# Kernel tuning notes

Hardware: AMD Instinct MI355X
Metric: run time of the kernel (lower is better)

Reference implementation:

```python
import jax, jax.numpy as jnp
import numpy as np

B, S, HMODEL = 2, 4096, 2048
NH, HD, K = 16, 128, 4
RMS_EPS = 1e-5
L2_EPS = 1e-6


def setup_inputs() -> dict:
    key = jax.random.key(0)
    ks = jax.random.split(key, 10)
    def p(k, shape, std=0.02):
        return jax.random.normal(k, shape, jnp.float32) * std
    return {
        "x": jax.random.normal(ks[0], (B, S, HMODEL), jnp.float32),
        "Wq": p(ks[1], (NH * HD, HMODEL)),
        "Wk": p(ks[2], (NH * HD, HMODEL)),
        "Wv": p(ks[3], (NH * HD, HMODEL)),
        "Wb": p(ks[4], (NH, HMODEL)),
        "Wo": p(ks[5], (HMODEL, NH * HD)),
        "conv_q": p(ks[6], (NH * HD, K), 0.3),
        "conv_k": p(ks[7], (NH * HD, K), 0.3),
        "conv_v": p(ks[8], (NH * HD, K), 0.3),
        "rms_w": jnp.ones((HD,), jnp.float32),
    }


def causal_conv_silu(x, w):
    # depthwise causal conv1d: x [B,S,C], w [C,K]; out[t] = sum_i w[:,i]*x[t-K+1+i]
    Kw = w.shape[1]
    xp = jnp.pad(x, ((0, 0), (Kw - 1, 0), (0, 0)))
    out = sum(w[:, i] * xp[:, i:i + x.shape[1], :] for i in range(Kw))
    return jax.nn.silu(out)


def l2norm(x):
    return x * jax.lax.rsqrt(jnp.sum(x * x, axis=-1, keepdims=True) + L2_EPS)


def reference(x, Wq, Wk, Wv, Wb, Wo, conv_q, conv_k, conv_v, rms_w):
    b, s, _ = x.shape
    nh = Wb.shape[0]
    hd = Wq.shape[0] // nh

    q = causal_conv_silu(x @ Wq.T, conv_q)
    k = causal_conv_silu(x @ Wk.T, conv_k)
    v = causal_conv_silu(x @ Wv.T, conv_v)

    q = q.reshape(b, s, nh, hd)
    k = k.reshape(b, s, nh, hd)
    v = v.reshape(b, s, nh, hd)
    beta = jax.nn.sigmoid(x @ Wb.T)  # [B,S,NH]

    # qk l2 norm in kernel + default scale d_k^-0.5 on q
    q = l2norm(q) * (hd ** -0.5)
    k = l2norm(k)

    # delta rule recurrence: state [B,NH,HD,HD] (d_k x d_v)
    qT = jnp.moveaxis(q, 1, 0)  # [S,B,NH,HD]
    kT = jnp.moveaxis(k, 1, 0)
    vT = jnp.moveaxis(v, 1, 0)
    bT = jnp.moveaxis(beta, 1, 0)  # [S,B,NH]

    def step(state, inp):
        qt, kt, vt, bt = inp
        pred = jnp.einsum('bhd,bhdv->bhv', kt, state)
        delta = bt[..., None] * (vt - pred)
        state = state + jnp.einsum('bhd,bhv->bhdv', kt, delta)
        ot = jnp.einsum('bhd,bhdv->bhv', qt, state)
        return state, ot

    s0 = jnp.zeros((b, nh, hd, hd), x.dtype)
    _, o = jax.lax.scan(step, s0, (qT, kT, vT, bT))
    o = jnp.moveaxis(o, 0, 1)  # [B,S,NH,HD]

    # RMSNorm over head_dim
    o = o * jax.lax.rsqrt(jnp.mean(o * o, axis=-1, keepdims=True) + RMS_EPS) * rms_w

    o = o.reshape(b, s, nh * hd) @ Wo.T
    return o
```

## Files before the change

### kernel.cpp

```cpp
#include <hip/hip_runtime.h>

#define DI __device__ __forceinline__

constexpr int Bb = 2, Ss = 4096, Hm = 2048, NHh = 16, HDd = 128;
constexpr int ROWS = Bb * Ss;
constexpr int QKVN = 3 * Hm;
constexpr int CC = 64;
constexpr int NC = Ss / CC;

typedef __bf16 bf16x8 __attribute__((ext_vector_type(8)));
typedef float f32x4 __attribute__((ext_vector_type(4)));

DI unsigned short f2bf(float f) {
  unsigned int u = __float_as_uint(f);
  u = u + 0x7FFFu + ((u >> 16) & 1u);
  return (unsigned short)(u >> 16);
}
DI float bf2f(unsigned int u) { return __uint_as_float(u << 16); }
DI void ld_bf8(const unsigned short* p, float* f) {
  uint4 u = *(const uint4*)p;
  f[0] = bf2f(u.x & 0xffffu); f[1] = bf2f(u.x >> 16);
  f[2] = bf2f(u.y & 0xffffu); f[3] = bf2f(u.y >> 16);
  f[4] = bf2f(u.z & 0xffffu); f[5] = bf2f(u.z >> 16);
  f[6] = bf2f(u.w & 0xffffu); f[7] = bf2f(u.w >> 16);
}

DI void gld16(const unsigned short* g, unsigned short* l) {
  __builtin_amdgcn_global_load_lds(
      (const __attribute__((address_space(1))) unsigned int*)g,
      (__attribute__((address_space(3))) unsigned int*)l, 16, 0, 0);
}

DI void bar_lds() {
  asm volatile("s_waitcnt lgkmcnt(0)" ::: "memory");
  __builtin_amdgcn_s_barrier();
}

__global__ void cast_x_k(const float* __restrict__ x, unsigned short* __restrict__ xb) {
  int i = blockIdx.x * 256 + threadIdx.x;
  float4 f = ((const float4*)x)[i];
  ushort4 u;
  u.x = f2bf(f.x); u.y = f2bf(f.y); u.z = f2bf(f.z); u.w = f2bf(f.w);
  ((ushort4*)xb)[i] = u;
}

__global__ void cast_w_k(const float* __restrict__ Wq, const float* __restrict__ Wk,
                         const float* __restrict__ Wv, const float* __restrict__ Wo,
                         unsigned short* __restrict__ wqkv, unsigned short* __restrict__ wo) {
  const int W1 = Hm * Hm;
  int idx = blockIdx.x * 256 + threadIdx.x;
  for (int r = 0; r < 4; r++) {
    int i = idx + r * W1;
    if (i < W1)            wqkv[i] = f2bf(Wq[i]);
    else if (i < 2 * W1)   wqkv[i] = f2bf(Wk[i - W1]);
    else if (i < 3 * W1)   wqkv[i] = f2bf(Wv[i - 2 * W1]);
    else                   wo[i - 3 * W1] = f2bf(Wo[i - 3 * W1]);
  }
}

DI bf16x8 ldsw(const unsigned short* base, int r, int c16) {
  return *(const bf16x8*)&base[r * 64 + ((c16 ^ (r & 7)) << 3)];
}

template <bool BF16_OUT>
__global__ __launch_bounds__(512) void gemm256(const unsigned short* __restrict__ A,
                                               const unsigned short* __restrict__ Bm,
                                               void* __restrict__ Cout,
                                               int M, int N, int Kd) {
  __shared__ __align__(16) unsigned short As[3][16384];
  __shared__ __align__(16) unsigned short Bs[2][16384];
  int tid = threadIdx.x;
  int wave = tid >> 6, lane = tid & 63;
  int lm = lane & 15, lq = lane >> 4;
  int wm = (wave >> 2) * 128, wn = (wave & 3) * 64;

  int nx = N >> 8;
  int nwg = gridDim.x * gridDim.y;
  int lin = blockIdx.x + gridDim.x * blockIdx.y;
  int cpx = nwg >> 3;
  int swz = (lin & 7) * cpx + (lin >> 3);
  int bn = (swz % nx) << 8, bm = (swz / nx) << 8;

  int NT = Kd >> 6;
  int rsub = lane >> 3;
  int csw = ((lane & 7) ^ rsub) << 3;

  auto stageA = [&](int buf, int half, int ts) {
    int ksrc = (ts < NT ? ts : NT - 1) << 6;
#pragma unroll
    for (int i = 0; i < 2; i++) {
      int blk = wave * 2 + i;
      int r = half * 128 + blk * 8 + rsub;
      gld16(&A[(size_t)(bm + r) * Kd + ksrc + csw], &As[buf][half * 8192 + blk * 512]);
    }
  };
  auto stageB = [&](int buf, int half, int ts) {
    int ksrc = (ts < NT ? ts : NT - 1) << 6;
#pragma unroll
    for (int i = 0; i < 2; i++) {
      int blk = wave * 2 + i;
      int r = half * 128 + blk * 8 + rsub;
      gld16(&Bm[(size_t)(bn + r) * Kd + ksrc + csw], &Bs[buf][half * 8192 + blk * 512]);
    }
  };

  f32x4 acc[8][4] = {};
  bf16x8 a[4][2], b[4][2];

  stageA(0, 0, 0); stageA(0, 1, 0); stageB(0, 0, 0); stageB(0, 1, 0);
  stageA(1, 0, 1); stageA(1, 1, 1); stageB(1, 0, 1); stageB(1, 1, 1);
  asm volatile("s_waitcnt vmcnt(8)" ::: "memory");
  __builtin_amdgcn_s_barrier();
#pragma unroll
  for (int fi = 0; fi < 4; fi++)
#pragma unroll
    for (int kk = 0; kk < 2; kk++)
      a[fi][kk] = ldsw(As[0], wm + fi * 16 + lm, kk * 4 + lq);
#pragma unroll
  for (int fj = 0; fj < 2; fj++)
#pragma unroll
    for (int kk = 0; kk < 2; kk++)
      b[fj][kk] = ldsw(Bs[0], wn + fj * 16 + lm, kk * 4 + lq);

  int cur_a = 0, cur_b = 0;
  for (int t = 0; t < NT; t++) {
    const unsigned short* Ac = As[cur_a];
    const unsigned short* Bc = Bs[cur_b];
    int nxt_a = cur_a == 2 ? 0 : cur_a + 1;
    const unsigned short* An = As[nxt_a];
    const unsigned short* Bn = Bs[cur_b ^ 1];
    int ap2 = cur_a == 0 ? 2 : cur_a - 1;

    asm volatile("" ::: "memory");
    __builtin_amdgcn_s_barrier();
    asm volatile("s_waitcnt lgkmcnt(0)" ::: "memory");
    __builtin_amdgcn_sched_barrier(0);
    __builtin_amdgcn_s_setprio(1);
#pragma unroll
    for (int fj = 0; fj < 2; fj++)
#pragma unroll
      for (int kk = 0; kk < 2; kk++)
        b[2 + fj][kk] = ldsw(Bc, wn + (2 + fj) * 16 + lm, kk * 4 + lq);
#pragma unroll
    for (int kk = 0; kk < 2; kk++)
#pragma unroll
      for (int fi = 0; fi < 4; fi++)
#pragma unroll
        for (int fj = 0; fj < 2; fj++)
          acc[fi][fj] = __builtin_amdgcn_mfma_f32_16x16x32_bf16(a[fi][kk], b[fj][kk], acc[fi][fj], 0, 0, 0);
    __builtin_amdgcn_s_setprio(0);
    stageA(ap2, 0, t + 2);

    asm volatile("" ::: "memory");
    __builtin_amdgcn_s_barrier();
    asm volatile("s_waitcnt lgkmcnt(0)" ::: "memory");
    __builtin_amdgcn_sched_barrier(0);
    __builtin_amdgcn_s_setprio(1);
#pragma unroll
    for (int fi = 0; fi < 4; fi++) {
#pragma unroll
      for (int kk = 0; kk < 2; kk++)
#pragma unroll
        for (int fj = 0; fj < 2; fj++)
          acc[fi][2 + fj] = __builtin_amdgcn_mfma_f32_16x16x32_bf16(a[fi][kk], b[2 + fj][kk], acc[fi][2 + fj], 0, 0, 0);
#pragma unroll
      for (int kk = 0; kk < 2; kk++)
        a[fi][kk] = ldsw(Ac, wm + 64 + fi * 16 + lm, kk * 4 + lq);
    }
    __builtin_amdgcn_s_setprio(0);
    stageA(ap2, 1, t + 2);

    asm volatile("" ::: "memory");
    __builtin_amdgcn_s_barrier();
    asm volatile("s_waitcnt lgkmcnt(0)" ::: "memory");
    __builtin_amdgcn_sched_barrier(0);
    __builtin_amdgcn_s_setprio(1);
#pragma unroll
    for (int kk = 0; kk < 2; kk++)
#pragma unroll
      for (int fi = 0; fi < 4; fi++)
#pragma unroll
        for (int fj = 0; fj < 2; fj++)
          acc[4 + fi][2 + fj] = __builtin_amdgcn_mfma_f32_16x16x32_bf16(a[fi][kk], b[2 + fj][kk], acc[4 + fi][2 + fj], 0, 0, 0);
    __builtin_amdgcn_s_setprio(0);
    stageB(cur_b, 0, t + 2);

    asm volatile("" ::: "memory");
    __builtin_amdgcn_s_barrier();
    asm volatile("s_waitcnt vmcnt(6) lgkmcnt(0)" ::: "memory");
    __builtin_amdgcn_sched_barrier(0);
    asm volatile("" ::: "memory");
    __builtin_amdgcn_s_barrier();
    __builtin_amdgcn_s_setprio(1);
#pragma unroll
    for (int fi = 0; fi < 4; fi++) {
#pragma unroll
      for (int kk = 0; kk < 2; kk++)
#pragma unroll
        for (int fj = 0; fj < 2; fj++)
          acc[4 + fi][fj] = __builtin_amdgcn_mfma_f32_16x16x32_bf16(a[fi][kk], b[fj][kk], acc[4 + fi][fj], 0, 0, 0);
#pragma unroll
      for (int kk = 0; kk < 2; kk++)
        a[fi][kk] = ldsw(An, wm + fi * 16 + lm, kk * 4 + lq);
    }
#pragma unroll
    for (int fj = 0; fj < 2; fj++)
#pragma unroll
      for (int kk = 0; kk < 2; kk++)
        b[fj][kk] = ldsw(Bn, wn + fj * 16 + lm, kk * 4 + lq);
    __builtin_amdgcn_s_setprio(0);
    stageB(cur_b, 1, t + 2);

    cur_a = nxt_a; cur_b ^= 1;
  }

#pragma unroll
  for (int fi = 0; fi < 8; fi++)
#pragma unroll
    for (int fj = 0; fj < 4; fj++) {
      int row = bm + wm + fi * 16 + lq * 4;
      int col = bn + wn + fj * 16 + lm;
#pragma unroll
      for (int r = 0; r < 4; r++) {
        if (BF16_OUT)
          ((unsigned short*)Cout)[(size_t)(row + r) * N + col] = f2bf(acc[fi][fj][r]);
        else
          ((float*)Cout)[(size_t)(row + r) * N + col] = acc[fi][fj][r];
      }
    }
}

__global__ __launch_bounds__(256) void conv_k(const unsigned short* __restrict__ qkvh,
                                              const float* __restrict__ cwq,
                                              const float* __restrict__ cwk,
                                              const float* __restrict__ cwv,
                                              unsigned short* __restrict__ qb,
                                              unsigned short* __restrict__ kb,
                                              unsigned short* __restrict__ vb) {
  __shared__ __align__(16) float sm[32 * 260];
  __shared__ float fac[64];
  int tid = threadIdx.x;
  int cblk = blockIdx.x * 256;
  int s0 = blockIdx.y * 32;
  int z = blockIdx.z;
  int sel = z >> 1, b = z & 1;
  const float* cw = sel == 0 ? cwq : (sel == 1 ? cwk : cwv);
  int c = cblk + tid;
  float4 w = ((const float4*)cw)[c];
  const unsigned short* in = qkvh + (size_t)b * Ss * QKVN + sel * Hm + c;
  float x0 = (s0 >= 3) ? bf2f(in[(size_t)(s0 - 3) * QKVN]) : 0.f;
  float x1 = (s0 >= 2) ? bf2f(in[(size_t)(s0 - 2) * QKVN]) : 0.f;
  float x2 = (s0 >= 1) ? bf2f(in[(size_t)(s0 - 1) * QKVN]) : 0.f;
  for (int si = 0; si < 32; si++) {
    float x3 = bf2f(in[(size_t)(s0 + si) * QKVN]);
    float a = w.x * x0 + w.y * x1 + w.z * x2 + w.w * x3;
    sm[si * 260 + tid] = a / (1.f + __expf(-a));
    x0 = x1; x1 = x2; x2 = x3;
  }
  __syncthreads();
  if (sel < 2) {
    int si = tid >> 3, p = tid & 7;
    const float* row = &sm[si * 260 + p * 32];
    float ss = 0.f;
#pragma unroll
    for (int j = 0; j < 32; j += 4) {
      float4 v4 = *(const float4*)(row + j);
      ss += v4.x * v4.x + v4.y * v4.y + v4.z * v4.z + v4.w * v4.w;
    }
    ss += __shfl_xor(ss, 1);
    ss += __shfl_xor(ss, 2);
    float f = rsqrtf(ss + 1e-6f);
    if (sel == 0) f *= 0.08838834764831845f;
    if ((p & 3) == 0) fac[si * 2 + (p >> 2)] = f;
  }
  __syncthreads();
  unsigned short* outp = sel == 0 ? qb : (sel == 1 ? kb : vb);
  int hl = tid >> 7;
  for (int si = 0; si < 32; si++) {
    float val = sm[si * 260 + tid];
    if (sel < 2) val *= fac[si * 2 + hl];
    outp[(size_t)(b * Ss + s0 + si) * Hm + cblk + tid] = f2bf(val);
  }
}

__global__ __launch_bounds__(256) void beta_k(const float* __restrict__ x,
                                              const float* __restrict__ Wbm,
                                              float* __restrict__ beta) {
  int wid = threadIdx.x >> 6, lane = threadIdx.x & 63;
  int row = blockIdx.x * 4 + wid;
  int h = lane & 15, part = lane >> 4;
  const float* xr = x + (size_t)row * Hm + part * 512;
  const float* wr = Wbm + (size_t)h * Hm + part * 512;
  float acc = 0.f;
  for (int j = 0; j < 512; j += 4) {
    float4 xv = *(const float4*)(xr + j);
    float4 wv = *(const float4*)(wr + j);
    acc += xv.x * wv.x + xv.y * wv.y + xv.z * wv.z + xv.w * wv.w;
  }
  acc += __shfl_xor(acc, 16);
  acc += __shfl_xor(acc, 32);
  if (part == 0) beta[(size_t)row * NHh + h] = 1.f / (1.f + __expf(-acc));
}

__global__ __launch_bounds__(256) void recA_k(const unsigned short* __restrict__ qg,
                                              unsigned short* kg,
                                              const unsigned short* __restrict__ vg,
                                              const float* __restrict__ beta,
                                              unsigned short* __restrict__ Wo_,
                                              unsigned short* __restrict__ Uo,
                                              unsigned short* __restrict__ Kto) {
  __shared__ __align__(16) unsigned short Kc[64 * 136];
  __shared__ __align__(16) unsigned short Qc[64 * 136];
  __shared__ __align__(16) unsigned short Vt[128 * 72];
  __shared__ __align__(16) unsigned short Kt[128 * 72];
  __shared__ __align__(16) unsigned short Xa[64 * 72], Xat[64 * 72];
  __shared__ __align__(16) unsigned short Xb2[64 * 72], Xbt[64 * 72];
  __shared__ __align__(16) unsigned short Pa[64 * 72], Pb[64 * 72];
  __shared__ float bl[64];
  int tid = threadIdx.x;
  int c = blockIdx.x, bh = blockIdx.y;
  int b = bh >> 4, h = bh & 15;
  size_t cid = (size_t)bh * NC + c;
  size_t rowbase = (size_t)b * Ss + (size_t)c * CC;
  int wave = tid >> 6, lane = tid & 63, lm = lane & 15, lq = lane >> 4;

  for (int idx = tid; idx < 1024; idx += 256) {
    int r = idx >> 4, c8 = (idx & 15) * 8;
    *(uint4*)&Kc[r * 136 + c8] = *(const uint4*)&kg[(rowbase + r) * Hm + h * HDd + c8];
    *(uint4*)&Qc[r * 136 + c8] = *(const uint4*)&qg[(rowbase + r) * Hm + h * HDd + c8];
  }
  for (int idx = tid; idx < 8192; idx += 256) {
    int s = idx >> 7, vv = idx & 127;
    Vt[vv * 72 + s] = vg[(rowbase + s) * Hm + h * HDd + vv];
  }
  if (tid < 64) bl[tid] = beta[(rowbase + tid) * NHh + h];
  __syncthreads();

  for (int idx = tid; idx < 8192; idx += 256) {
    int s = idx >> 7, d = idx & 127;
    Kt[d * 72 + s] = Kc[s * 136 + d];
  }
  {
    f32x4 accA[4] = {};
#pragma unroll
    for (int kk = 0; kk < 4; kk++) {
      bf16x8 af = *(const bf16x8*)&Kc[(wave * 16 + lm) * 136 + kk * 32 + lq * 8];
#pragma unroll
      for (int st = 0; st < 4; st++) {
        bf16x8 bfr = *(const bf16x8*)&Kc[(st * 16 + lm) * 136 + kk * 32 + lq * 8];
        accA[st] = __builtin_amdgcn_mfma_f32_16x16x32_bf16(af, bfr, accA[st], 0, 0, 0);
      }
    }
#pragma unroll
    for (int st = 0; st < 4; st++)
#pragma unroll
      for (int r = 0; r < 4; r++) {
        int t = wave * 16 + lq * 4 + r, s = st * 16 + lm;
        float m = (t > s) ? -bl[t] * accA[st][r] : 0.f;
        unsigned short mb = f2bf(m);
        Xa[t * 72 + s] = mb;
        Xat[s * 72 + t] = mb;
        Pa[t * 72 + s] = (t == s) ? f2bf(1.f) : mb;
      }
  }
  {
    f32x4 accQ[4] = {};
#pragma unroll
    for (int kk = 0; kk < 4; kk++) {
      bf16x8 af = *(const bf16x8*)&Qc[(wave * 16 + lm) * 136 + kk * 32 + lq * 8];
#pragma unroll
      for (int st = 0; st < 4; st++) {
        bf16x8 bfr = *(const bf16x8*)&Kc[(st * 16 + lm) * 136 + kk * 32 + lq * 8];
        accQ[st] = __builtin_amdgcn_mfma_f32_16x16x32_bf16(af, bfr, accQ[st], 0, 0, 0);
      }
    }
#pragma unroll
    for (int st = 0; st < 4; st++)
#pragma unroll
      for (int r = 0; r < 4; r++) {
        int t = wave * 16 + lq * 4 + r, s = st * 16 + lm;
        kg[(rowbase + t) * Hm + h * HDd + s] = (s <= t) ? f2bf(accQ[st][r]) : (unsigned short)0;
      }
  }
  __syncthreads();

  unsigned short *X = Xa, *Xt = Xat, *Xn = Xb2, *Xnt = Xbt, *P = Pa, *Pn = Pb;
  for (int lvl = 1; lvl <= 5; lvl++) {
    f32x4 a1[4] = {}, a2[4] = {};
#pragma unroll
    for (int kk = 0; kk < 2; kk++) {
      bf16x8 afx  = *(const bf16x8*)&X[(wave * 16 + lm) * 72 + kk * 32 + lq * 8];
      bf16x8 afxt = *(const bf16x8*)&Xt[(wave * 16 + lm) * 72 + kk * 32 + lq * 8];
#pragma unroll
      for (int st = 0; st < 4; st++) {
        bf16x8 bx  = *(const bf16x8*)&X[(st * 16 + lm) * 72 + kk * 32 + lq * 8];
        bf16x8 bxt = *(const bf16x8*)&Xt[(st * 16 + lm) * 72 + kk * 32 + lq * 8];
        a1[st] = __builtin_amdgcn_mfma_f32_16x16x32_bf16(afx, bxt, a1[st], 0, 0, 0);
        a2[st] = __builtin_amdgcn_mfma_f32_16x16x32_bf16(afxt, bx, a2[st], 0, 0, 0);
      }
    }
#pragma unroll
    for (int st = 0; st < 4; st++)
#pragma unroll
      for (int r = 0; r < 4; r++) {
        int t = wave * 16 + lq * 4 + r, s = st * 16 + lm;
        Xn[t * 72 + s]  = f2bf(a1[st][r]);
        Xnt[t * 72 + s] = f2bf(a2[st][r]);
      }
    __syncthreads();
    f32x4 ap[4];
#pragma unroll
    for (int st = 0; st < 4; st++)
#pragma unroll
      for (int r = 0; r < 4; r++)
        ap[st][r] = bf2f(P[(wave * 16 + lq * 4 + r) * 72 + st * 16 + lm]);
#pragma unroll
    for (int kk = 0; kk < 2; kk++) {
      bf16x8 afp = *(const bf16x8*)&P[(wave * 16 + lm) * 72 + kk * 32 + lq * 8];
#pragma unroll
      for (int st = 0; st < 4; st++) {
        bf16x8 bxnt = *(const bf16x8*)&Xnt[(st * 16 + lm) * 72 + kk * 32 + lq * 8];
        ap[st] = __builtin_amdgcn_mfma_f32_16x16x32_bf16(afp, bxnt, ap[st], 0, 0, 0);
      }
    }
#pragma unroll
    for (int st = 0; st < 4; st++)
#pragma unroll
      for (int r = 0; r < 4; r++) {
        int t = wave * 16 + lq * 4 + r, s = st * 16 + lm;
        Pn[t * 72 + s] = f2bf((lvl == 5) ? ap[st][r] * bl[s] : ap[st][r]);
      }
    unsigned short* tmp;
    tmp = X; X = Xn; Xn = tmp;
    tmp = Xt; Xt = Xnt; Xnt = tmp;
    tmp = P; P = Pn; Pn = tmp;
    __syncthreads();
  }

  for (int idx = tid; idx < 1024; idx += 256) {
    int d = idx >> 3, s8 = (idx & 7) * 8;
    *(uint4*)&Kto[cid * 8192 + d * 64 + s8] = *(const uint4*)&Kt[d * 72 + s8];
  }
  {
    unsigned short* Up = Uo + cid * 8192;
    unsigned short* Wp = Wo_ + cid * 8192;
    f32x4 accU[8] = {}, accW[8] = {};
#pragma unroll
    for (int kk = 0; kk < 2; kk++) {
      bf16x8 af = *(const bf16x8*)&P[(wave * 16 + lm) * 72 + kk * 32 + lq * 8];
#pragma unroll
      for (int nt = 0; nt < 8; nt++) {
        bf16x8 bv = *(const bf16x8*)&Vt[(nt * 16 + lm) * 72 + kk * 32 + lq * 8];
        bf16x8 bk = *(const bf16x8*)&Kt[(nt * 16 + lm) * 72 + kk * 32 + lq * 8];
        accU[nt] = __builtin_amdgcn_mfma_f32_16x16x32_bf16(af, bv, accU[nt], 0, 0, 0);
        accW[nt] = __builtin_amdgcn_mfma_f32_16x16x32_bf16(af, bk, accW[nt], 0, 0, 0);
      }
    }
#pragma unroll
    for (int nt = 0; nt < 8; nt++)
#pragma unroll
      for (int r = 0; r < 4; r++) {
        int t = wave * 16 + lq * 4 + r, n = nt * 16 + lm;
        Up[t * 128 + n] = f2bf(accU[nt][r]);
        Wp[t * 128 + n] = f2bf(accW[nt][r]);
      }
  }
}

__global__ __launch_bounds__(256) void recB_k(const unsigned short* __restrict__ qg,
                                              const unsigned short* __restrict__ atg,
                                              const unsigned short* __restrict__ Wg,
                                              const unsigned short* __restrict__ Ug,
                                              const unsigned short* __restrict__ Ktg,
                                              unsigned short* __restrict__ og) {
  __shared__ __align__(16) unsigned short Wc[64 * 136];
  __shared__ __align__(16) unsigned short Qc[64 * 136];
  __shared__ __align__(16) unsigned short Ktc[128 * 72];
  __shared__ __align__(16) unsigned short Atc[64 * 72];
  __shared__ __align__(16) unsigned short Uc[64 * 24];
  __shared__ __align__(16) unsigned short Dt[16 * 72];
  __shared__ __align__(16) unsigned short Stb[16 * 136];
  __shared__ float St32[16 * 132];
  int tid = threadIdx.x;
  int lin = blockIdx.x + (blockIdx.y << 3);
  int xcd = lin & 7, slot = lin >> 3;
  int vs = slot & 7;
  int bh = xcd + ((slot >> 3) << 3);
  int b = bh >> 4, h = bh & 15, v0 = vs * 16;
  int wave = tid >> 6, lane = tid & 63, lm = lane & 15, lq = lane >> 4;

  for (int i = tid; i < 16 * 132; i += 256) St32[i] = 0.f;
  for (int i = tid; i < 16 * 136; i += 256) Stb[i] = 0;

  {
    size_t cid0 = (size_t)bh * NC;
    size_t rb0 = (size_t)b * Ss;
    const unsigned short* Wp = Wg + cid0 * 8192;
    const unsigned short* Ktp = Ktg + cid0 * 8192;
    const unsigned short* Up = Ug + cid0 * 8192 + v0;
#pragma unroll
    for (int j = 0; j < 4; j++) {
      int idx = tid + j * 256;
      int r = idx >> 4, c8 = (idx & 15) * 8;
      *(uint4*)&Wc[r * 136 + c8] = *(const uint4*)&Wp[r * 128 + c8];
      *(uint4*)&Qc[r * 136 + c8] = *(const uint4*)&qg[(rb0 + r) * Hm + h * HDd + c8];
      int r2 = idx >> 3, d8 = (idx & 7) * 8;
      *(uint4*)&Ktc[r2 * 72 + d8] = *(const uint4*)&Ktp[r2 * 64 + d8];
    }
#pragma unroll
    for (int j = 0; j < 2; j++) {
      int idx = tid + j * 256;
      int t = idx >> 3, s8 = (idx & 7) * 8;
      *(uint4*)&Atc[t * 72 + s8] = *(const uint4*)&atg[(rb0 + t) * Hm + h * HDd + s8];
    }
    if (tid < 128) {
      int t = tid >> 1, c8 = (tid & 1) * 8;
      *(uint4*)&Uc[t * 24 + c8] = *(const uint4*)&Up[t * 128 + c8];
    }
  }
  __syncthreads();

  for (int c = 0; c < NC; c++) {
    size_t rb = (size_t)b * Ss + (size_t)c * CC;
    int cn = (c + 1 < NC) ? c + 1 : c;
    size_t cidn = (size_t)bh * NC + cn;
    size_t rbn = (size_t)b * Ss + (size_t)cn * CC;
    const unsigned short* Wpn = Wg + cidn * 8192;
    const unsigned short* Ktpn = Ktg + cidn * 8192;
    const unsigned short* Upn = Ug + cidn * 8192 + v0;
    uint4 pw[4], pq[4], pk[4], pa[2], pu;
#pragma unroll
    for (int j = 0; j < 4; j++) {
      int idx = tid + j * 256;
      int r = idx >> 4, c8 = (idx & 15) * 8;
      pw[j] = *(const uint4*)&Wpn[r * 128 + c8];
      pq[j] = *(const uint4*)&qg[(rbn + r) * Hm + h * HDd + c8];
      int r2 = idx >> 3, d8 = (idx & 7) * 8;
      pk[j] = *(const uint4*)&Ktpn[r2 * 64 + d8];
    }
#pragma unroll
    for (int j = 0; j < 2; j++) {
      int idx = tid + j * 256;
      int t = idx >> 3, s8 = (idx & 7) * 8;
      pa[j] = *(const uint4*)&atg[(rbn + t) * Hm + h * HDd + s8];
    }
    if (tid < 128) {
      int t = tid >> 1, c8 = (tid & 1) * 8;
      pu = *(const uint4*)&Upn[t * 128 + c8];
    }

    {
      f32x4 accD = {};
#pragma unroll
      for (int kk = 0; kk < 4; kk++) {
        bf16x8 af = *(const bf16x8*)&Wc[(wave * 16 + lm) * 136 + kk * 32 + lq * 8];
        bf16x8 bfr = *(const bf16x8*)&Stb[lm * 136 + kk * 32 + lq * 8];
        accD = __builtin_amdgcn_mfma_f32_16x16x32_bf16(af, bfr, accD, 0, 0, 0);
      }
#pragma unroll
      for (int r = 0; r < 4; r++) {
        int t = wave * 16 + lq * 4 + r;
        float dv = bf2f(Uc[t * 24 + lm]) - accD[r];
        Dt[lm * 72 + t] = f2bf(dv);
      }
    }
    bar_lds();

    f32x4 accO = {};
    f32x4 accP[2] = {};
    {
#pragma unroll
      for (int kk = 0; kk < 4; kk++) {
        bf16x8 af = *(const bf16x8*)&Qc[(wave * 16 + lm) * 136 + kk * 32 + lq * 8];
        bf16x8 bfr = *(const bf16x8*)&Stb[lm * 136 + kk * 32 + lq * 8];
        accO = __builtin_amdgcn_mfma_f32_16x16x32_bf16(af, bfr, accO, 0, 0, 0);
      }
#pragma unroll
      for (int kk = 0; kk < 2; kk++) {
        bf16x8 af = *(const bf16x8*)&Atc[(wave * 16 + lm) * 72 + kk * 32 + lq * 8];
        bf16x8 bfr = *(const bf16x8*)&Dt[lm * 72 + kk * 32 + lq * 8];
        accO = __builtin_amdgcn_mfma_f32_16x16x32_bf16(af, bfr, accO, 0, 0, 0);
        bf16x8 afd = *(const bf16x8*)&Dt[lm * 72 + kk * 32 + lq * 8];
#pragma unroll
        for (int j = 0; j < 2; j++) {
          int dt = wave * 2 + j;
          bf16x8 bk = *(const bf16x8*)&Ktc[(dt * 16 + lm) * 72 + kk * 32 + lq * 8];
          accP[j] = __builtin_amdgcn_mfma_f32_16x16x32_bf16(afd, bk, accP[j], 0, 0, 0);
        }
      }
    }
    bar_lds();

#pragma unroll
    for (int r = 0; r < 4; r++) {
      int t = wave * 16 + lq * 4 + r;
      og[(rb + t) * Hm + h * HDd + v0 + lm] = f2bf(accO[r]);
    }
#pragma unroll
    for (int j = 0; j < 2; j++) {
      int dt = wave * 2 + j;
#pragma unroll
      for (int r = 0; r < 4; r++) {
        int vv = lq * 4 + r, d = dt * 16 + lm;
        float ns = St32[vv * 132 + d] + accP[j][r];
        St32[vv * 132 + d] = ns;
        Stb[vv * 136 + d] = f2bf(ns);
      }
    }
#pragma unroll
    for (int j = 0; j < 4; j++) {
      int idx = tid + j * 256;
      int r = idx >> 4, c8 = (idx & 15) * 8;
      *(uint4*)&Wc[r * 136 + c8] = pw[j];
      *(uint4*)&Qc[r * 136 + c8] = pq[j];
      int r2 = idx >> 3, d8 = (idx & 7) * 8;
      *(uint4*)&Ktc[r2 * 72 + d8] = pk[j];
    }
#pragma unroll
    for (int j = 0; j < 2; j++) {
      int idx = tid + j * 256;
      int t = idx >> 3, s8 = (idx & 7) * 8;
      *(uint4*)&Atc[t * 72 + s8] = pa[j];
    }
    if (tid < 128) {
      int t = tid >> 1, c8 = (tid & 1) * 8;
      *(uint4*)&Uc[t * 24 + c8] = pu;
    }
    bar_lds();
  }
}

__global__ __launch_bounds__(256) void rmsn_k(const unsigned short* __restrict__ o,
                                              const float* __restrict__ rw,
                                              unsigned short* __restrict__ ob) {
  int tid = threadIdx.x;
  size_t rowoff = (size_t)blockIdx.x * Hm + tid * 8;
  float f[8];
  ld_bf8(o + rowoff, f);
  float ss = f[0]*f[0] + f[1]*f[1] + f[2]*f[2] + f[3]*f[3] +
             f[4]*f[4] + f[5]*f[5] + f[6]*f[6] + f[7]*f[7];
  ss += __shfl_xor(ss, 1); ss += __shfl_xor(ss, 2); ss += __shfl_xor(ss, 4); ss += __shfl_xor(ss, 8);
  float sc = rsqrtf(ss * (1.f / 128.f) + 1e-5f);
  int d = (tid & 15) * 8;
  float4 wa = *(const float4*)(rw + d);
  float4 wb = *(const float4*)(rw + d + 4);
  ushort4 u0, u1;
  u0.x = f2bf(f[0] * sc * wa.x); u0.y = f2bf(f[1] * sc * wa.y);
  u0.z = f2bf(f[2] * sc * wa.z); u0.w = f2bf(f[3] * sc * wa.w);
  u1.x = f2bf(f[4] * sc * wb.x); u1.y = f2bf(f[5] * sc * wb.y);
  u1.z = f2bf(f[6] * sc * wb.z); u1.w = f2bf(f[7] * sc * wb.w);
  ((ushort4*)ob)[rowoff / 4] = u0;
  ((ushort4*)ob)[rowoff / 4 + 1] = u1;
}

extern "C" void kernel_launch(void* const* d_in, const int* in_sizes, int n_in,
                              void* d_out, int out_size, void* d_ws, size_t ws_size,
                              hipStream_t stream) {
  const float* x  = (const float*)d_in[0];
  const float* Wq = (const float*)d_in[1];
  const float* Wk = (const float*)d_in[2];
  const float* Wv = (const float*)d_in[3];
  const float* Wb = (const float*)d_in[4];
  const float* Wo = (const float*)d_in[5];
  const float* cq = (const float*)d_in[6];
  const float* ck = (const float*)d_in[7];
  const float* cv = (const float*)d_in[8];
  const float* rw = (const float*)d_in[9];

  unsigned short* xb  = (unsigned short*)d_out;
  unsigned short* vb  = (unsigned short*)d_out + (size_t)ROWS * Hm;
  unsigned short* o_b = (unsigned short*)d_out;
  float* out = (float*)d_out;

  char* ws = (char*)d_ws;
  size_t off = 0;
  auto alloc = [&](size_t bytes) {
    void* p = ws + off;
    off = (off + bytes + 255) & ~(size_t)255;
    return p;
  };
  unsigned short* wqkv = (unsigned short*)alloc((size_t)QKVN * Hm * 2);
  unsigned short* wob  = (unsigned short*)alloc((size_t)Hm * Hm * 2);
  unsigned short* qkvh = (unsigned short*)alloc((size_t)ROWS * QKVN * 2);
  unsigned short* qb   = (unsigned short*)alloc((size_t)ROWS * Hm * 2);
  unsigned short* kb   = (unsigned short*)alloc((size_t)ROWS * Hm * 2);
  float* beta          = (float*)alloc((size_t)ROWS * NHh * 4);
  unsigned short* Wch = qkvh;
  unsigned short* Uch = qkvh + (size_t)2048 * 8192;
  unsigned short* Kth = qkvh + (size_t)2 * 2048 * 8192;
  unsigned short* obb = qkvh;

  cast_x_k<<<ROWS * Hm / 1024, 256, 0, stream>>>(x, xb);
  cast_w_k<<<Hm * Hm / 256, 256, 0, stream>>>(Wq, Wk, Wv, Wo, wqkv, wob);
  gemm256<true><<<dim3(QKVN / 256, ROWS / 256), 512, 0, stream>>>(xb, wqkv, qkvh, ROWS, QKVN, Hm);
  beta_k<<<ROWS / 4, 256, 0, stream>>>(x, Wb, beta);
  conv_k<<<dim3(Hm / 256, Ss / 32, Bb * 3), 256, 0, stream>>>(qkvh, cq, ck, cv, qb, kb, vb);
  recA_k<<<dim3(NC, 32), 256, 0, stream>>>(qb, kb, vb, beta, Wch, Uch, Kth);
  recB_k<<<dim3(8, 32), 256, 0, stream>>>(qb, kb, Wch, Uch, Kth, o_b);
  rmsn_k<<<ROWS, 256, 0, stream>>>(o_b, rw, obb);
  gemm256<false><<<dim3(Hm / 256, ROWS / 256), 512, 0, stream>>>(obb, wob, out, ROWS, Hm, Hm);
}
```

Baseline: 934.0 us.

## Shrink recA shared memory via buffer aliasing to fit two blocks per CU

Replaces the separate shared arrays in recA_k with one aliased byte buffer. Q and transposed V share storage, Kt reuses the X buffers after the doubling loop, and P is updated in place. The row stride drops from 72 to 68, V is staged through registers instead of a strided global gather, the last-level X product is skipped, and the kernel is marked for two blocks per CU via launch_bounds. The goal is higher occupancy and less global and LDS traffic, at the cost of more complex barrier ordering and possible LDS bank conflicts from the 68 stride.

Measured after the change: 1.003 ms. 7.4% more time.

```diff
diff --git a/kernel.cpp b/kernel.cpp
--- a/kernel.cpp
+++ b/kernel.cpp
@@ -302,21 +302,24 @@
   if (part == 0) beta[(size_t)row * NHh + h] = 1.f / (1.f + __expf(-acc));
 }
 
-__global__ __launch_bounds__(256) void recA_k(const unsigned short* __restrict__ qg,
+__global__ __launch_bounds__(256, 2) void recA_k(const unsigned short* __restrict__ qg,
                                               unsigned short* kg,
                                               const unsigned short* __restrict__ vg,
                                               const float* __restrict__ beta,
                                               unsigned short* __restrict__ Wo_,
                                               unsigned short* __restrict__ Uo,
                                               unsigned short* __restrict__ Kto) {
-  __shared__ __align__(16) unsigned short Kc[64 * 136];
-  __shared__ __align__(16) unsigned short Qc[64 * 136];
-  __shared__ __align__(16) unsigned short Vt[128 * 72];
-  __shared__ __align__(16) unsigned short Kt[128 * 72];
-  __shared__ __align__(16) unsigned short Xa[64 * 72], Xat[64 * 72];
-  __shared__ __align__(16) unsigned short Xb2[64 * 72], Xbt[64 * 72];
-  __shared__ __align__(16) unsigned short Pa[64 * 72], Pb[64 * 72];
-  __shared__ float bl[64];
+  __shared__ __align__(16) char smem[78592];
+  unsigned short* Kc  = (unsigned short*)(smem);
+  unsigned short* QV  = (unsigned short*)(smem + 17408);
+  unsigned short* Xa_ = (unsigned short*)(smem + 34816);
+  unsigned short* Xat_= (unsigned short*)(smem + 43520);
+  unsigned short* Xb2_= (unsigned short*)(smem + 52224);
+  unsigned short* Xbt_= (unsigned short*)(smem + 60928);
+  unsigned short* Ktl = (unsigned short*)(smem + 34816);
+  unsigned short* Pa  = (unsigned short*)(smem + 69632);
+  float* bl           = (float*)(smem + 78336);
+
   int tid = threadIdx.x;
   int c = blockIdx.x, bh = blockIdx.y;
   int b = bh >> 4, h = bh & 15;
@@ -324,22 +327,18 @@
   size_t rowbase = (size_t)b * Ss + (size_t)c * CC;
   int wave = tid >> 6, lane = tid & 63, lm = lane & 15, lq = lane >> 4;
 
-  for (int idx = tid; idx < 1024; idx += 256) {
+  uint4 vr[4];
+#pragma unroll
+  for (int j = 0; j < 4; j++) {
+    int idx = tid + j * 256;
     int r = idx >> 4, c8 = (idx & 15) * 8;
     *(uint4*)&Kc[r * 136 + c8] = *(const uint4*)&kg[(rowbase + r) * Hm + h * HDd + c8];
-    *(uint4*)&Qc[r * 136 + c8] = *(const uint4*)&qg[(rowbase + r) * Hm + h * HDd + c8];
-  }
-  for (int idx = tid; idx < 8192; idx += 256) {
-    int s = idx >> 7, vv = idx & 127;
-    Vt[vv * 72 + s] = vg[(rowbase + s) * Hm + h * HDd + vv];
+    *(uint4*)&QV[r * 136 + c8] = *(const uint4*)&qg[(rowbase + r) * Hm + h * HDd + c8];
+    vr[j] = *(const uint4*)&vg[(rowbase + r) * Hm + h * HDd + c8];
   }
   if (tid < 64) bl[tid] = beta[(rowbase + tid) * NHh + h];
-  __syncthreads();
-
-  for (int idx = tid; idx < 8192; idx += 256) {
-    int s = idx >> 7, d = idx & 127;
-    Kt[d * 72 + s] = Kc[s * 136 + d];
-  }
+  bar_lds();
+
   {
     f32x4 accA[4] = {};
 #pragma unroll
@@ -358,16 +357,16 @@
         int t = wave * 16 + lq * 4 + r, s = st * 16 + lm;
         float m = (t > s) ? -bl[t] * accA[st][r] : 0.f;
         unsigned short mb = f2bf(m);
-        Xa[t * 72 + s] = mb;
-        Xat[s * 72 + t] = mb;
-        Pa[t * 72 + s] = (t == s) ? f2bf(1.f) : mb;
+        Xa_[t * 68 + s] = mb;
+        Xat_[s * 68 + t] = mb;
+        Pa[t * 68 + s] = (t == s) ? f2bf(1.f) : mb;
       }
   }
   {
     f32x4 accQ[4] = {};
 #pragma unroll
     for (int kk = 0; kk < 4; kk++) {
-      bf16x8 af = *(const bf16x8*)&Qc[(wave * 16 + lm) * 136 + kk * 32 + lq * 8];
+      bf16x8 af = *(const bf16x8*)&QV[(wave * 16 + lm) * 136 + kk * 32 + lq * 8];
 #pragma unroll
       for (int st = 0; st < 4; st++) {
         bf16x8 bfr = *(const bf16x8*)&Kc[(st * 16 + lm) * 136 + kk * 32 + lq * 8];
@@ -382,20 +381,30 @@
         kg[(rowbase + t) * Hm + h * HDd + s] = (s <= t) ? f2bf(accQ[st][r]) : (unsigned short)0;
       }
   }
-  __syncthreads();
-
-  unsigned short *X = Xa, *Xt = Xat, *Xn = Xb2, *Xnt = Xbt, *P = Pa, *Pn = Pb;
+  bar_lds();
+
+#pragma unroll
+  for (int j = 0; j < 4; j++) {
+    int idx = tid + j * 256;
+    int r = idx >> 4, c8 = (idx & 15) * 8;
+    const unsigned short* pv = (const unsigned short*)&vr[j];
+#pragma unroll
+    for (int e = 0; e < 8; e++) QV[(c8 + e) * 68 + r] = pv[e];
+  }
+
+  unsigned short *X = Xa_, *Xt = Xat_, *Xn = Xb2_, *Xnt = Xbt_;
   for (int lvl = 1; lvl <= 5; lvl++) {
     f32x4 a1[4] = {}, a2[4] = {};
 #pragma unroll
     for (int kk = 0; kk < 2; kk++) {
-      bf16x8 afx  = *(const bf16x8*)&X[(wave * 16 + lm) * 72 + kk * 32 + lq * 8];
-      bf16x8 afxt = *(const bf16x8*)&Xt[(wave * 16 + lm) * 72 + kk * 32 + lq * 8];
+      bf16x8 afx  = *(const bf16x8*)&X[(wave * 16 + lm) * 68 + kk * 32 + lq * 8];
+      bf16x8 afxt = *(const bf16x8*)&Xt[(wave * 16 + lm) * 68 + kk * 32 + lq * 8];
 #pragma unroll
       for (int st = 0; st < 4; st++) {
-        bf16x8 bx  = *(const bf16x8*)&X[(st * 16 + lm) * 72 + kk * 32 + lq * 8];
-        bf16x8 bxt = *(const bf16x8*)&Xt[(st * 16 + lm) * 72 + kk * 32 + lq * 8];
-        a1[st] = __builtin_amdgcn_mfma_f32_16x16x32_bf16(afx, bxt, a1[st], 0, 0, 0);
+        bf16x8 bx  = *(const bf16x8*)&X[(st * 16 + lm) * 68 + kk * 32 + lq * 8];
+        bf16x8 bxt = *(const bf16x8*)&Xt[(st * 16 + lm) * 68 + kk * 32 + lq * 8];
+        if (lvl < 5)
+          a1[st] = __builtin_amdgcn_mfma_f32_16x16x32_bf16(afx, bxt, a1[st], 0, 0, 0);
         a2[st] = __builtin_amdgcn_mfma_f32_16x16x32_bf16(afxt, bx, a2[st], 0, 0, 0);
       }
     }
@@ -404,42 +413,49 @@
 #pragma unroll
       for (int r = 0; r < 4; r++) {
         int t = wave * 16 + lq * 4 + r, s = st * 16 + lm;
-        Xn[t * 72 + s]  = f2bf(a1[st][r]);
-        Xnt[t * 72 + s] = f2bf(a2[st][r]);
-      }
-    __syncthreads();
+        if (lvl < 5) Xn[t * 68 + s] = f2bf(a1[st][r]);
+        Xnt[t * 68 + s] = f2bf(a2[st][r]);
+      }
     f32x4 ap[4];
 #pragma unroll
     for (int st = 0; st < 4; st++)
 #pragma unroll
       for (int r = 0; r < 4; r++)
-        ap[st][r] = bf2f(P[(wave * 16 + lq * 4 + r) * 72 + st * 16 + lm]);
-#pragma unroll
-    for (int kk = 0; kk < 2; kk++) {
-      bf16x8 afp = *(const bf16x8*)&P[(wave * 16 + lm) * 72 + kk * 32 + lq * 8];
+        ap[st][r] = bf2f(Pa[(wave * 16 + lq * 4 + r) * 68 + st * 16 + lm]);
+    bf16x8 afp[2];
+#pragma unroll
+    for (int kk = 0; kk < 2; kk++)
+      afp[kk] = *(const bf16x8*)&Pa[(wave * 16 + lm) * 68 + kk * 32 + lq * 8];
+    bar_lds();
+#pragma unroll
+    for (int kk = 0; kk < 2; kk++)
 #pragma unroll
       for (int st = 0; st < 4; st++) {
-        bf16x8 bxnt = *(const bf16x8*)&Xnt[(st * 16 + lm) * 72 + kk * 32 + lq * 8];
-        ap[st] = __builtin_amdgcn_mfma_f32_16x16x32_bf16(afp, bxnt, ap[st], 0, 0, 0);
-      }
-    }
+        bf16x8 bxnt = *(const bf16x8*)&Xnt[(st * 16 + lm) * 68 + kk * 32 + lq * 8];
+        ap[st] = __builtin_amdgcn_mfma_f32_16x16x32_bf16(afp[kk], bxnt, ap[st], 0, 0, 0);
+      }
 #pragma unroll
     for (int st = 0; st < 4; st++)
 #pragma unroll
       for (int r = 0; r < 4; r++) {
         int t = wave * 16 + lq * 4 + r, s = st * 16 + lm;
-        Pn[t * 72 + s] = f2bf((lvl == 5) ? ap[st][r] * bl[s] : ap[st][r]);
-      }
+        Pa[t * 68 + s] = f2bf((lvl == 5) ? ap[st][r] * bl[s] : ap[st][r]);
+      }
+    bar_lds();
     unsigned short* tmp;
     tmp = X; X = Xn; Xn = tmp;
     tmp = Xt; Xt = Xnt; Xnt = tmp;
-    tmp = P; P = Pn; Pn = tmp;
-    __syncthreads();
-  }
+  }
+
+  for (int idx = tid; idx < 8192; idx += 256) {
+    int s = idx >> 7, d = idx & 127;
+    Ktl[d * 68 + s] = Kc[s * 136 + d];
+  }
+  bar_lds();
 
   for (int idx = tid; idx < 1024; idx += 256) {
     int d = idx >> 3, s8 = (idx & 7) * 8;
-    *(uint4*)&Kto[cid * 8192 + d * 64 + s8] = *(const uint4*)&Kt[d * 72 + s8];
+    *(uint4*)&Kto[cid * 8192 + d * 64 + s8] = *(const uint4*)&Ktl[d * 68 + s8];
   }
   {
     unsigned short* Up = Uo + cid * 8192;
@@ -447,11 +463,11 @@
     f32x4 accU[8] = {}, accW[8] = {};
 #pragma unroll
     for (int kk = 0; kk < 2; kk++) {
-      bf16x8 af = *(const bf16x8*)&P[(wave * 16 + lm) * 72 + kk * 32 + lq * 8];
+      bf16x8 af = *(const bf16x8*)&Pa[(wave * 16 + lm) * 68 + kk * 32 + lq * 8];
 #pragma unroll
       for (int nt = 0; nt < 8; nt++) {
-        bf16x8 bv = *(const bf16x8*)&Vt[(nt * 16 + lm) * 72 + kk * 32 + lq * 8];
-        bf16x8 bk = *(const bf16x8*)&Kt[(nt * 16 + lm) * 72 + kk * 32 + lq * 8];
+        bf16x8 bv = *(const bf16x8*)&QV[(nt * 16 + lm) * 68 + kk * 32 + lq * 8];
+        bf16x8 bk = *(const bf16x8*)&Ktl[(nt * 16 + lm) * 68 + kk * 32 + lq * 8];
         accU[nt] = __builtin_amdgcn_mfma_f32_16x16x32_bf16(af, bv, accU[nt], 0, 0, 0);
         accW[nt] = __builtin_amdgcn_mfma_f32_16x16x32_bf16(af, bk, accW[nt], 0, 0, 0);
       }
```
